# Kernel tuning notes

Measured on AMD Instinct MI355X. Metric: run time of the kernel, lower is better.

The kernel has to match this reference:

```python
import jax, jax.numpy as jnp
import numpy as np

HIDDEN = 512
ATTEN = 512
BATCH = 32
STEP = 2048


def setup_inputs() -> dict:
    key = jax.random.key(0)
    k1, k2, k3, k4, k5 = jax.random.split(key, 5)
    nn_outs = jax.random.normal(k1, (BATCH, STEP, HIDDEN), dtype=jnp.float32)
    # variable lengths in [1, STEP]
    batch_lens = jnp.clip(
        jax.random.randint(k2, (BATCH,), 0, STEP + 1), 1, STEP
    ).astype(jnp.int64)
    # Linear(hidden_dim, atten_dim): W [hidden, atten], b [atten]
    W = jax.random.normal(k3, (HIDDEN, ATTEN), dtype=jnp.float32) / np.sqrt(HIDDEN)
    b = jnp.zeros((ATTEN,), dtype=jnp.float32)
    # context parameter uniform(-0.1, 0.1)
    context = jax.random.uniform(k4, (ATTEN,), dtype=jnp.float32, minval=-0.1, maxval=0.1)
    return {"nn_outs": nn_outs, "batch_lens": batch_lens, "W": W, "b": b, "context": context}


def reference(nn_outs, batch_lens, W, b, context):
    # proj = tanh(Linear(nn_outs))  -> [B, S, A]
    proj = jnp.tanh(jnp.einsum("bsh,ha->bsa", nn_outs, W) + b)
    # scores = proj @ context       -> [B, S]
    scores = jnp.einsum("bsa,a->bs", proj, context)
    # masked softmax over valid positions only (per-sample variable length)
    mask = jnp.arange(scores.shape[1])[None, :] < batch_lens[:, None]  # [B, S]
    scores = jnp.where(mask, scores, -jnp.inf)
    atten = jax.nn.softmax(scores, axis=-1)  # padded positions get weight 0
    # weighted sum over time -> [B, H]
    return jnp.einsum("bs,bsh->bh", atten, nn_outs)
```

## Files before the change

### kernel.cpp

```cpp
#include <hip/hip_runtime.h>
#include <hip/hip_bf16.h>
#include <math.h>

#define HIDDEN 512
#define ATTEN  512
#define BATCH  32
#define STEP   2048

#define BM 128
#define BN 256
#define NS (ATTEN / BN)
#define BK 32
#define NT (HIDDEN / BK)
#define THREADS 512
#define NTILES (BATCH * (STEP / BM) * NS)
#define NBLOCKS 512

#define NCH 32
#define CHS (STEP / NCH)

typedef __attribute__((ext_vector_type(8))) short bf16x8;
typedef __attribute__((ext_vector_type(4))) float f32x4;

__device__ __forceinline__ long long load_len(const int* lens_raw, int b) {
    bool is64 = (lens_raw[1] == 0);
    if (is64) return ((const long long*)lens_raw)[b];
    return (long long)lens_raw[b];
}

__device__ __forceinline__ short f2bf(float x) {
    unsigned u = __float_as_uint(x);
    unsigned r = (u + 0x7FFFu + ((u >> 16) & 1u)) >> 16;
    return (short)r;
}

__device__ __forceinline__ float fast_tanh(float x) {
    float e = __expf(2.0f * x);
    return 1.0f - 2.0f / (e + 1.0f);
}

__global__ __launch_bounds__(512) void wsplit_kernel(
    const float* __restrict__ W, short* __restrict__ wglds, int* __restrict__ ctr)
{
    if (blockIdx.x == 0 && threadIdx.x == 0) *ctr = 0;
    int a = blockIdx.x;
    int h = threadIdx.x;
    float v = W[(size_t)h * ATTEN + a];
    short hi = f2bf(v);
    int ns = a >> 8, c = a & 255;
    int kt = h >> 5, s = (h >> 3) & 3, j = h & 7;
    int r2 = c >> 1;
    int slot8 = (((c & 1) << 2) | s) ^ (r2 & 7);
    size_t tb = ((size_t)ns * NT + kt) * 1024;
    wglds[(tb + (size_t)r2 * 8 + slot8) * 8 + j] = hi;
}

__global__ __launch_bounds__(THREADS, 4) void scores_mfma_kernel(
    const float* __restrict__ X,
    const int*   __restrict__ lens_raw,
    const short* __restrict__ wglds,
    const float* __restrict__ bias,
    const float* __restrict__ ctx,
    float* __restrict__ scores_part,
    int* __restrict__ ctr)
{
    __shared__ char smem[48 * 1024];
    char* const At = smem;
    char* const B0 = smem + 16 * 1024;
    char* const B1 = smem + 32 * 1024;
    __shared__ int widx;

    int t = threadIdx.x;
    int wave = t >> 6, lane = t & 63;
    int wrow = wave >> 2, wcol = wave & 3;
    int l15 = lane & 15, l4 = lane >> 4;
    int ar = t >> 2, aq = t & 3;
    int wvuni16 = (t & ~63) * 16;

    for (;;) {
        __syncthreads();
        if (t == 0) widx = atomicAdd(ctr, 1);
        __syncthreads();
        int idx = widx;
        if (idx >= NTILES) break;

        int ns = idx & 1;
        int mt = idx >> 1;
        int b  = mt >> 4;
        int s0 = (mt & 15) * BM;
        long long len = load_len(lens_raw, b);
        if ((long long)s0 >= len) continue;

        int ko = (idx * 7) & (NT - 1);

        const float* xrow = X + ((size_t)b * STEP + s0 + ar) * HIDDEN + aq * 8;
        const short* wbase = wglds + (size_t)ns * NT * 1024 * 8;

        f32x4 acc[4][4];
#pragma unroll
        for (int mi = 0; mi < 4; ++mi)
#pragma unroll
            for (int ni = 0; ni < 4; ++ni)
                acc[mi][ni] = (f32x4){0.f, 0.f, 0.f, 0.f};

        float4 px0, px1;

#define PXLOAD(KG)                                                           \
    do {                                                                     \
        px0 = *(const float4*)(xrow + (KG) * BK);                            \
        px1 = *(const float4*)(xrow + (KG) * BK + 4);                        \
    } while (0)

#define BISSUE(KG, SB)                                                       \
    do {                                                                     \
        _Pragma("unroll")                                                    \
        for (int i = 0; i < 2; ++i) {                                        \
            const short* g = wbase + ((size_t)(KG) * 1024 + i * 512 + t) * 8;\
            char* l = (SB) + i * 512 * 16 + wvuni16;                         \
            __builtin_amdgcn_global_load_lds(                                \
                (const __attribute__((address_space(1))) unsigned int*)g,    \
                (__attribute__((address_space(3))) unsigned int*)l,          \
                16, 0, 0);                                                   \
        }                                                                    \
    } while (0)

#define AWRITE()                                                             \
    do {                                                                     \
        float xs[8] = {px0.x, px0.y, px0.z, px0.w, px1.x, px1.y, px1.z, px1.w};\
        bf16x8 hv;                                                           \
        _Pragma("unroll")                                                    \
        for (int j = 0; j < 8; ++j) hv[j] = f2bf(xs[j]);                     \
        int rx = ar & 7;                                                     \
        *(bf16x8*)(At + ar * 128 + (((aq) ^ rx) << 4)) = hv;                 \
    } while (0)

#define COMPUTE(SB)                                                          \
    do {                                                                     \
        bf16x8 ah[4];                                                        \
        _Pragma("unroll")                                                    \
        for (int mi = 0; mi < 4; ++mi) {                                     \
            int row = wrow * 64 + mi * 16 + l15;                             \
            int rx = row & 7;                                                \
            ah[mi] = *(const bf16x8*)(At + row * 128 + ((l4 ^ rx) << 4));    \
        }                                                                    \
        _Pragma("unroll")                                                    \
        for (int ni = 0; ni < 4; ++ni) {                                     \
            int col = wcol * 64 + ni * 16 + l15;                             \
            int r2 = col >> 1;                                               \
            int sl = ((((col & 1) << 2) | l4) ^ (r2 & 7));                   \
            bf16x8 bh = *(const bf16x8*)((SB) + r2 * 128 + (sl << 4));       \
            _Pragma("unroll")                                                \
            for (int mi = 0; mi < 4; ++mi) {                                 \
                acc[mi][ni] = __builtin_amdgcn_mfma_f32_16x16x32_bf16(       \
                    ah[mi], bh, acc[mi][ni], 0, 0, 0);                       \
            }                                                                \
        }                                                                    \
    } while (0)

        PXLOAD(ko);
        BISSUE(ko, B0);
        AWRITE();
        __syncthreads();

#pragma unroll
        for (int kt = 0; kt < NT; ++kt) {
            int knxt = (ko + kt + 1) & (NT - 1);
            if (kt + 1 < NT) {
                PXLOAD(knxt);
                BISSUE(knxt, ((kt + 1) & 1) ? B1 : B0);
            }
            COMPUTE((kt & 1) ? B1 : B0);
            __syncthreads();
            if (kt + 1 < NT) {
                AWRITE();
                __syncthreads();
            }
        }
#undef PXLOAD
#undef BISSUE
#undef AWRITE
#undef COMPUTE

        float bi[4], ci[4];
#pragma unroll
        for (int ni = 0; ni < 4; ++ni) {
            int a = ns * BN + wcol * 64 + ni * 16 + l15;
            bi[ni] = bias[a];
            ci[ni] = ctx[a];
        }
        float* partial = (float*)At;
#pragma unroll
        for (int mi = 0; mi < 4; ++mi) {
#pragma unroll
            for (int reg = 0; reg < 4; ++reg) {
                float s = 0.f;
#pragma unroll
                for (int ni = 0; ni < 4; ++ni)
                    s += fast_tanh(acc[mi][ni][reg] + bi[ni]) * ci[ni];
                s += __shfl_xor(s, 1);
                s += __shfl_xor(s, 2);
                s += __shfl_xor(s, 4);
                s += __shfl_xor(s, 8);
                if (l15 == 0) {
                    int row = wrow * 64 + mi * 16 + l4 * 4 + reg;
                    partial[wcol * BM + row] = s;
                }
            }
        }
        __syncthreads();
        if (t < BM) {
            float v = partial[0 * BM + t] + partial[1 * BM + t]
                    + partial[2 * BM + t] + partial[3 * BM + t];
            scores_part[((size_t)ns * BATCH + b) * STEP + s0 + t] = v;
        }
    }
}

__global__ __launch_bounds__(256) void wsum_kernel(
    const float* __restrict__ X, const int* __restrict__ lens_raw,
    const float* __restrict__ p0, const float* __restrict__ p1,
    float* __restrict__ partial)
{
    __shared__ float wmax[4], wsumr[4];
    __shared__ float ex[STEP];
    int ch = blockIdx.x;
    int b  = blockIdx.y;
    long long len = load_len(lens_raw, b);
    int t = threadIdx.x;

    const float* r0 = p0 + (size_t)b * STEP;
    const float* r1 = p1 + (size_t)b * STEP;
    float sv[STEP / 256];
    float locmax = -INFINITY;
#pragma unroll
    for (int k = 0; k < 8; ++k) {
        int s = t + k * 256;
        float v = ((long long)s < len) ? (r0[s] + r1[s]) : -INFINITY;
        sv[k] = v;
        locmax = fmaxf(locmax, v);
    }
    for (int o = 1; o < 64; o <<= 1) locmax = fmaxf(locmax, __shfl_xor(locmax, o));
    int wave = t >> 6, lane = t & 63;
    if (lane == 0) wmax[wave] = locmax;
    __syncthreads();
    float gmax = fmaxf(fmaxf(wmax[0], wmax[1]), fmaxf(wmax[2], wmax[3]));

    float ev[8];
    float locsum = 0.f;
#pragma unroll
    for (int k = 0; k < 8; ++k) {
        float e = (sv[k] == -INFINITY) ? 0.f : expf(sv[k] - gmax);
        ev[k] = e;
        locsum += e;
    }
    for (int o = 1; o < 64; o <<= 1) locsum += __shfl_xor(locsum, o);
    if (lane == 0) wsumr[wave] = locsum;
    __syncthreads();
    float inv = 1.f / (wsumr[0] + wsumr[1] + wsumr[2] + wsumr[3]);
#pragma unroll
    for (int k = 0; k < 8; ++k) ex[t + k * 256] = ev[k] * inv;
    __syncthreads();

    int s0 = ch * CHS;
    long long send_ll = (long long)(s0 + CHS);
    if (send_ll > len) send_ll = len;
    int send = (int)send_ll;

    const float* xbase = X + ((size_t)b * STEP) * HIDDEN + 2 * t;
    float2 a0v = {0.f, 0.f}, a1v = {0.f, 0.f};
    float2 a2v = {0.f, 0.f}, a3v = {0.f, 0.f};
    int s = s0;
    for (; s + 4 <= send; s += 4) {
        float w0 = ex[s], w1 = ex[s + 1], w2 = ex[s + 2], w3 = ex[s + 3];
        float2 x0 = *(const float2*)(xbase + (size_t)s * HIDDEN);
        float2 x1 = *(const float2*)(xbase + (size_t)(s + 1) * HIDDEN);
        float2 x2 = *(const float2*)(xbase + (size_t)(s + 2) * HIDDEN);
        float2 x3 = *(const float2*)(xbase + (size_t)(s + 3) * HIDDEN);
        a0v.x = fmaf(w0, x0.x, a0v.x); a0v.y = fmaf(w0, x0.y, a0v.y);
        a1v.x = fmaf(w1, x1.x, a1v.x); a1v.y = fmaf(w1, x1.y, a1v.y);
        a2v.x = fmaf(w2, x2.x, a2v.x); a2v.y = fmaf(w2, x2.y, a2v.y);
        a3v.x = fmaf(w3, x3.x, a3v.x); a3v.y = fmaf(w3, x3.y, a3v.y);
    }
    for (; s < send; ++s) {
        float w0 = ex[s];
        float2 x0 = *(const float2*)(xbase + (size_t)s * HIDDEN);
        a0v.x = fmaf(w0, x0.x, a0v.x); a0v.y = fmaf(w0, x0.y, a0v.y);
    }
    float2 acc = {(a0v.x + a1v.x) + (a2v.x + a3v.x),
                  (a0v.y + a1v.y) + (a2v.y + a3v.y)};
    float* prow = partial + ((size_t)b * NCH + ch) * HIDDEN;
    *(float2*)(prow + 2 * t) = acc;
}

__global__ __launch_bounds__(256) void finalize_kernel(
    const float* __restrict__ partial, float* __restrict__ out)
{
    int b = blockIdx.x;
    int t = threadIdx.x;
    float2 a = {0.f, 0.f};
#pragma unroll
    for (int ch = 0; ch < NCH; ++ch) {
        const float* prow = partial + ((size_t)b * NCH + ch) * HIDDEN;
        float2 v = *(const float2*)(prow + 2 * t);
        a.x += v.x;
        a.y += v.y;
    }
    *(float2*)(out + (size_t)b * HIDDEN + 2 * t) = a;
}

extern "C" void kernel_launch(void* const* d_in, const int* in_sizes, int n_in,
                              void* d_out, int out_size, void* d_ws, size_t ws_size,
                              hipStream_t stream) {
    const float* X    = (const float*)d_in[0];
    const int*   lens = (const int*)d_in[1];
    const float* W    = (const float*)d_in[2];
    const float* bias = (const float*)d_in[3];
    const float* ctx  = (const float*)d_in[4];
    float* out = (float*)d_out;

    char* ws = (char*)d_ws;
    float* sp      = (float*)ws;
    float* partial = (float*)(ws + 512 * 1024);
    short* wglds   = (short*)(ws + 2560 * 1024);
    int*   ctr     = (int*)(ws + 3072 * 1024);

    wsplit_kernel<<<dim3(ATTEN), 512, 0, stream>>>(W, wglds, ctr);
    scores_mfma_kernel<<<dim3(NBLOCKS), THREADS, 0, stream>>>(
        X, lens, wglds, bias, ctx, sp, ctr);
    wsum_kernel<<<dim3(NCH, BATCH), 256, 0, stream>>>(
        X, lens, sp, sp + (size_t)BATCH * STEP, partial);
    finalize_kernel<<<dim3(BATCH), 256, 0, stream>>>(partial, out);
}
```

Measured before the change: 83.71 us.

## Stream fp32 activations directly to LDS and convert to bf16 at fragment load

The activation tile now travels from global memory into double-buffered LDS as raw fp32 through global_load_lds, using an XOR-swizzled source address. The register staging, the software bf16 conversion and the extra barrier each k-step are removed. Conversion now happens when MFMA fragments are read, using the packed v_cvt_pk_bf16_f32 instruction. LDS use grows from 48KB to 64KB per block and each wave does more LDS reads, which could reduce how many blocks fit per CU.

```diff
diff --git a/kernel.cpp b/kernel.cpp
--- a/kernel.cpp
+++ b/kernel.cpp
@@ -32,6 +32,12 @@
     unsigned u = __float_as_uint(x);
     unsigned r = (u + 0x7FFFu + ((u >> 16) & 1u)) >> 16;
     return (short)r;
+}
+
+__device__ __forceinline__ unsigned cvtpk(float lo, float hi) {
+    unsigned r;
+    asm("v_cvt_pk_bf16_f32 %0, %1, %2" : "=v"(r) : "v"(lo), "v"(hi));
+    return r;
 }
 
 __device__ __forceinline__ float fast_tanh(float x) {
@@ -64,17 +70,17 @@
     float* __restrict__ scores_part,
     int* __restrict__ ctr)
 {
-    __shared__ char smem[48 * 1024];
-    char* const At = smem;
-    char* const B0 = smem + 16 * 1024;
-    char* const B1 = smem + 32 * 1024;
+    __shared__ char smem[64 * 1024];
+    char* const A0 = smem;
+    char* const A1 = smem + 16 * 1024;
+    char* const B0 = smem + 32 * 1024;
+    char* const B1 = smem + 48 * 1024;
     __shared__ int widx;
 
     int t = threadIdx.x;
     int wave = t >> 6, lane = t & 63;
     int wrow = wave >> 2, wcol = wave & 3;
     int l15 = lane & 15, l4 = lane >> 4;
-    int ar = t >> 2, aq = t & 3;
     int wvuni16 = (t & ~63) * 16;
 
     for (;;) {
@@ -93,7 +99,7 @@
 
         int ko = (idx * 7) & (NT - 1);
 
-        const float* xrow = X + ((size_t)b * STEP + s0 + ar) * HIDDEN + aq * 8;
+        const float* xbase = X + ((size_t)b * STEP + s0) * HIDDEN;
         const short* wbase = wglds + (size_t)ns * NT * 1024 * 8;
 
         f32x4 acc[4][4];
@@ -103,12 +109,20 @@
             for (int ni = 0; ni < 4; ++ni)
                 acc[mi][ni] = (f32x4){0.f, 0.f, 0.f, 0.f};
 
-        float4 px0, px1;
-
-#define PXLOAD(KG)                                                           \
+#define ADMA(KG, SA)                                                         \
     do {                                                                     \
-        px0 = *(const float4*)(xrow + (KG) * BK);                            \
-        px1 = *(const float4*)(xrow + (KG) * BK + 4);                        \
+        _Pragma("unroll")                                                    \
+        for (int i = 0; i < 2; ++i) {                                        \
+            int n = t + i * 512;                                             \
+            int row = n >> 3, q = n & 7;                                     \
+            int qg = q ^ (row & 7);                                          \
+            const float* g = xbase + (size_t)row * HIDDEN + (KG) * BK + qg * 4; \
+            char* l = (SA) + i * 8192 + wvuni16;                             \
+            __builtin_amdgcn_global_load_lds(                                \
+                (const __attribute__((address_space(1))) unsigned int*)g,    \
+                (__attribute__((address_space(3))) unsigned int*)l,          \
+                16, 0, 0);                                                   \
+        }                                                                    \
     } while (0)
 
 #define BISSUE(KG, SB)                                                       \
@@ -124,24 +138,23 @@
         }                                                                    \
     } while (0)
 
-#define AWRITE()                                                             \
-    do {                                                                     \
-        float xs[8] = {px0.x, px0.y, px0.z, px0.w, px1.x, px1.y, px1.z, px1.w};\
-        bf16x8 hv;                                                           \
-        _Pragma("unroll")                                                    \
-        for (int j = 0; j < 8; ++j) hv[j] = f2bf(xs[j]);                     \
-        int rx = ar & 7;                                                     \
-        *(bf16x8*)(At + ar * 128 + (((aq) ^ rx) << 4)) = hv;                 \
-    } while (0)
-
-#define COMPUTE(SB)                                                          \
+#define COMPUTE(SA, SB)                                                      \
     do {                                                                     \
         bf16x8 ah[4];                                                        \
         _Pragma("unroll")                                                    \
         for (int mi = 0; mi < 4; ++mi) {                                     \
             int row = wrow * 64 + mi * 16 + l15;                             \
             int rx = row & 7;                                                \
-            ah[mi] = *(const bf16x8*)(At + row * 128 + ((l4 ^ rx) << 4));    \
+            f32x4 va = *(const f32x4*)((SA) + row * 128                      \
+                                       + (((2 * l4) ^ rx) << 4));            \
+            f32x4 vb = *(const f32x4*)((SA) + row * 128                      \
+                                       + (((2 * l4 + 1) ^ rx) << 4));        \
+            unsigned d0 = cvtpk(va[0], va[1]);                               \
+            unsigned d1 = cvtpk(va[2], va[3]);                               \
+            unsigned d2 = cvtpk(vb[0], vb[1]);                               \
+            unsigned d3 = cvtpk(vb[2], vb[3]);                               \
+            uint4 u = {d0, d1, d2, d3};                                      \
+            ah[mi] = *(bf16x8*)&u;                                           \
         }                                                                    \
         _Pragma("unroll")                                                    \
         for (int ni = 0; ni < 4; ++ni) {                                     \
@@ -157,28 +170,23 @@
         }                                                                    \
     } while (0)
 
-        PXLOAD(ko);
+        ADMA(ko, A0);
         BISSUE(ko, B0);
-        AWRITE();
         __syncthreads();
 
 #pragma unroll
-        for (int kt = 0; kt < NT; ++kt) {
-            int knxt = (ko + kt + 1) & (NT - 1);
-            if (kt + 1 < NT) {
-                PXLOAD(knxt);
-                BISSUE(knxt, ((kt + 1) & 1) ? B1 : B0);
+        for (int i = 0; i < NT; ++i) {
+            int kn = (ko + i + 1) & (NT - 1);
+            if (i + 1 < NT) {
+                if (((i + 1) & 1)) { ADMA(kn, A1); BISSUE(kn, B1); }
+                else               { ADMA(kn, A0); BISSUE(kn, B0); }
             }
-            COMPUTE((kt & 1) ? B1 : B0);
+            if ((i & 1) == 0) COMPUTE(A0, B0);
+            else              COMPUTE(A1, B1);
             __syncthreads();
-            if (kt + 1 < NT) {
-                AWRITE();
-                __syncthreads();
-            }
         }
-#undef PXLOAD
+#undef ADMA
 #undef BISSUE
-#undef AWRITE
 #undef COMPUTE
 
         float bi[4], ci[4];
@@ -188,7 +196,7 @@
             bi[ni] = bias[a];
             ci[ni] = ctx[a];
         }
-        float* partial = (float*)At;
+        float* partial = (float*)A0;
 #pragma unroll
         for (int mi = 0; mi < 4; ++mi) {
 #pragma unroll
```

Result: no change. 84.05 us (+0.4%).
